# Performance work log

Measured on AMD Instinct MI355X. Metric: run time of the kernel, lower is better.

The kernel has to match this reference:

```python
import jax, jax.numpy as jnp
import numpy as np

B, N, K = 2, 8192, 9
FEAT, COST = 128, 128
LEAKY = 0.1
BN_EPS = 1e-5


def setup_inputs() -> dict:
    key = jax.random.key(0)
    ks = iter(jax.random.split(key, 64))

    def nrm(shape, s=0.05):
        return jax.random.normal(next(ks), shape, jnp.float32) * s

    inp = {
        "xyz": nrm((B, 3, N), 1.0),
        "feats": nrm((B, FEAT, N), 1.0),
        "cost_volume": nrm((B, COST, N), 1.0),
        "flow": nrm((B, 3, N), 1.0),
    }
    cin = FEAT + COST + 3  # feats + cost + flow channels = 259
    for i, (ci, co) in enumerate([(cin + 3, 128), (128 + 3, 128)]):
        p = f"pc{i}_"
        inp[p + "wn_w0"] = nrm((8, 3)); inp[p + "wn_b0"] = nrm((8,))
        inp[p + "wn_w1"] = nrm((8, 8)); inp[p + "wn_b1"] = nrm((8,))
        inp[p + "wn_w2"] = nrm((16, 8)); inp[p + "wn_b2"] = nrm((16,))
        inp[p + "lin_w"] = nrm((co, 16 * ci)); inp[p + "lin_b"] = nrm((co,))
        inp[p + "bn_g"] = 1.0 + nrm((co,)); inp[p + "bn_b"] = nrm((co,))
        inp[p + "bn_m"] = nrm((co,))
        inp[p + "bn_v"] = jax.random.uniform(next(ks), (co,), jnp.float32, 0.5, 1.5)
    inp["mlp0_w"] = nrm((128, 128)); inp["mlp0_b"] = nrm((128,))
    inp["mlp1_w"] = nrm((64, 128)); inp["mlp1_b"] = nrm((64,))
    inp["fc_w"] = nrm((3, 64)); inp["fc_b"] = nrm((3,))
    return inp


def _leaky(x):
    return jnp.where(x > 0, x, LEAKY * x)


def _pointconv(xyz, pts, wn, lin_w, lin_b, bn):
    # xyz: [B,N,3], pts: [B,N,D]
    Bn, Nn, _ = xyz.shape
    sq = jnp.sum(xyz * xyz, -1)
    # squared pairwise distances [B,N,N]
    d = sq[:, :, None] + sq[:, None, :] - 2.0 * jnp.einsum('bnc,bmc->bnm', xyz, xyz)
    _, idx = jax.lax.top_k(-d, K)  # K nearest neighbors, [B,N,K]
    gat = jax.vmap(lambda p, i: p[i])
    gxyz = gat(xyz, idx)                       # [B,N,K,3]
    norm = gxyz - xyz[:, :, None, :]           # relative coords
    gpts = gat(pts, idx)                       # [B,N,K,D]
    feat = jnp.concatenate([norm, gpts], -1)   # [B,N,K,C]
    w = norm
    for W, b in wn:  # WeightNet: 1x1 convs == per-neighbor MLP, ReLU
        w = jax.nn.relu(jnp.einsum('bnki,oi->bnko', w, W) + b)
    # aggregate: [B,N,C,K] @ [B,N,K,16] -> [B,N,C*16]
    agg = jnp.einsum('bnkc,bnkw->bncw', feat, w).reshape(Bn, Nn, -1)
    y = agg @ lin_w.T + lin_b
    g, bb, m, v = bn  # BatchNorm1d eval mode
    y = (y - m) * (g / jnp.sqrt(v + BN_EPS)) + bb
    return _leaky(y)


def reference(xyz, feats, cost_volume, flow,
              pc0_wn_w0, pc0_wn_b0, pc0_wn_w1, pc0_wn_b1, pc0_wn_w2, pc0_wn_b2,
              pc0_lin_w, pc0_lin_b, pc0_bn_g, pc0_bn_b, pc0_bn_m, pc0_bn_v,
              pc1_wn_w0, pc1_wn_b0, pc1_wn_w1, pc1_wn_b1, pc1_wn_w2, pc1_wn_b2,
              pc1_lin_w, pc1_lin_b, pc1_bn_g, pc1_bn_b, pc1_bn_m, pc1_bn_v,
              mlp0_w, mlp0_b, mlp1_w, mlp1_b, fc_w, fc_b):
    xyz_t = xyz.transpose(0, 2, 1)  # [B,N,3]
    pts = jnp.concatenate([feats, cost_volume, flow], 1).transpose(0, 2, 1)  # [B,N,259]
    pts = _pointconv(xyz_t, pts,
                     [(pc0_wn_w0, pc0_wn_b0), (pc0_wn_w1, pc0_wn_b1), (pc0_wn_w2, pc0_wn_b2)],
                     pc0_lin_w, pc0_lin_b, (pc0_bn_g, pc0_bn_b, pc0_bn_m, pc0_bn_v))
    pts = _pointconv(xyz_t, pts,
                     [(pc1_wn_w0, pc1_wn_b0), (pc1_wn_w1, pc1_wn_b1), (pc1_wn_w2, pc1_wn_b2)],
                     pc1_lin_w, pc1_lin_b, (pc1_bn_g, pc1_bn_b, pc1_bn_m, pc1_bn_v))
    pts = _leaky(pts @ mlp0_w.T + mlp0_b)
    pts = _leaky(pts @ mlp1_w.T + mlp1_b)
    fl = pts @ fc_w.T + fc_b
    return (pts.transpose(0, 2, 1), jnp.clip(fl, -200.0, 200.0).transpose(0, 2, 1))
```

## Files before the change

### kernel.cpp

```cpp
#include <hip/hip_runtime.h>
#include <hip/hip_bf16.h>
#include <stdint.h>

#define NPTS 8192
#define NB 2

typedef unsigned int uint32;
typedef unsigned long long u64;
typedef unsigned short u16;
typedef short short8 __attribute__((ext_vector_type(8)));
typedef float f32x4 __attribute__((ext_vector_type(4)));

#define WB_IDX9  6291456u
#define WB_NORM  7077888u
#define WB_WT    9175040u
#define WB_PTS1  19660800u
#define WB_PTS2  28049408u
#define WB_L0BF  36438016u
#define WB_L0LO  37519360u
#define WB_L1BF  38600704u
#define WB_L1LO  39141376u
#define WB_W0BF  39682048u
#define WB_W0LO  39714816u
#define WB_W1BF  39747584u
#define WB_W1LO  39763968u
#define WB_BN    39780352u
#define WB_KEYS  19660800u

__device__ __forceinline__ u16 f2bf(float x) {
  uint32 u = __float_as_uint(x);
  u += 0x7fffu + ((u >> 16) & 1u);
  return (u16)(u >> 16);
}
__device__ __forceinline__ float bf2f(u16 h) { return __uint_as_float((uint32)h << 16); }
__device__ __forceinline__ float lrelu(float x) { return x > 0.f ? x : 0.1f * x; }
__device__ __forceinline__ uint32 ford(float d) {
  uint32 u = __float_as_uint(d);
  return (u & 0x80000000u) ? ~u : (u | 0x80000000u);
}
__device__ __forceinline__ float unford(uint32 o) {
  return (o & 0x80000000u) ? __uint_as_float(o & 0x7FFFFFFFu) : __uint_as_float(~o);
}
__device__ __forceinline__ float sq3n(float x, float y, float z) {
  return __fadd_rn(__fadd_rn(__fmul_rn(x, x), __fmul_rn(y, y)), __fmul_rn(z, z));
}

__global__ void k_prep(const float* __restrict__ L0, const float* __restrict__ L1,
                       const float* __restrict__ W0, const float* __restrict__ W1,
                       const float* __restrict__ lb0, const float* __restrict__ g0,
                       const float* __restrict__ bb0, const float* __restrict__ m0,
                       const float* __restrict__ v0,
                       const float* __restrict__ lb1, const float* __restrict__ g1,
                       const float* __restrict__ bb1, const float* __restrict__ m1,
                       const float* __restrict__ v1,
                       u16* __restrict__ L0bf, u16* __restrict__ L0lo,
                       u16* __restrict__ L1bf, u16* __restrict__ L1lo,
                       u16* __restrict__ W0bf, u16* __restrict__ W0lo,
                       u16* __restrict__ W1bf, u16* __restrict__ W1lo,
                       float* __restrict__ bn) {
  int i = blockIdx.x * 256 + threadIdx.x;
  if (i < 128 * 4224) {
    int o = i / 4224, kk = i % 4224;
    float w = kk < 4192 ? L0[o * 4192 + kk] : 0.f;
    u16 h = f2bf(w);
    L0bf[i] = h;
    L0lo[i] = f2bf(w - bf2f(h));
    return;
  }
  i -= 128 * 4224;
  if (i < 128 * 2112) {
    int o = i / 2112, kk = i % 2112;
    float w = kk < 2096 ? L1[o * 2096 + kk] : 0.f;
    u16 h = f2bf(w);
    L1bf[i] = h;
    L1lo[i] = f2bf(w - bf2f(h));
    return;
  }
  i -= 128 * 2112;
  if (i < 16384) {
    float w = W0[i];
    u16 h = f2bf(w);
    W0bf[i] = h;
    W0lo[i] = f2bf(w - bf2f(h));
    return;
  }
  i -= 16384;
  if (i < 8192) {
    float w = W1[i];
    u16 h = f2bf(w);
    W1bf[i] = h;
    W1lo[i] = f2bf(w - bf2f(h));
    return;
  }
  i -= 8192;
  if (i < 256) {
    int layer = i >> 7, o = i & 127;
    if (layer == 0) {
      float s = g0[o] / sqrtf(v0[o] + 1e-5f);
      bn[o] = s;
      bn[128 + o] = (lb0[o] - m0[o]) * s + bb0[o];
    } else {
      float s = g1[o] / sqrtf(v1[o] + 1e-5f);
      bn[256 + o] = s;
      bn[384 + o] = (lb1[o] - m1[o]) * s + bb1[o];
    }
  }
}

__global__ __launch_bounds__(256, 2) void k_knn(const float* __restrict__ xyz,
                                                u64* __restrict__ keys) {
  __shared__ float4 cand[1024];
  int bid = blockIdx.x;
  int b = bid >> 8;
  int qt = (bid >> 3) & 31;
  int ch = bid & 7;
  const float* xb = xyz + b * 3 * NPTS;
  int c0 = ch * 1024;
  for (int t = threadIdx.x; t < 1024; t += 256) {
    int j = c0 + t;
    float x = xb[j], y = xb[NPTS + j], z = xb[2 * NPTS + j];
    cand[t] = make_float4(x, y, z, sq3n(x, y, z));
  }
  __syncthreads();
  int q = qt * 256 + threadIdx.x;
  float qx = xb[q], qy = xb[NPTS + q], qz = xb[2 * NPTS + q];
  float sqq = sq3n(qx, qy, qz);
  u64 s[10];
#pragma unroll
  for (int i = 0; i < 10; i++) s[i] = ~0ull;
#pragma unroll 2
  for (int j = 0; j < 1024; j++) {
    float4 c = cand[j];
    float dot = __fadd_rn(__fadd_rn(__fmul_rn(qx, c.x), __fmul_rn(qy, c.y)),
                          __fmul_rn(qz, c.z));
    float d = __fsub_rn(__fadd_rn(sqq, c.w), __fmul_rn(2.0f, dot));
    u64 key = ((u64)ford(d) << 13) | (uint32)(c0 + j);
    if (key < s[9]) {
      s[9] = key;
#pragma unroll
      for (int t = 9; t > 0; --t) {
        u64 a = s[t - 1], bq = s[t];
        s[t - 1] = a < bq ? a : bq;
        s[t] = a < bq ? bq : a;
      }
    }
  }
  u64* dst = keys + ((size_t)(b * NPTS + q) * 8 + ch) * 10;
#pragma unroll
  for (int i = 0; i < 10; i++) dst[i] = s[i];
}

__global__ __launch_bounds__(256) void k_merge(const u64* __restrict__ keys,
                                               int* __restrict__ idx9) {
  int t = blockIdx.x * 256 + threadIdx.x;
  const u64* src = keys + (size_t)t * 80;
  u64 s[10];
#pragma unroll
  for (int i = 0; i < 10; i++) s[i] = ~0ull;
  for (int g = 0; g < 8; g++) {
#pragma unroll
    for (int i = 0; i < 10; i++) {
      u64 k = src[g * 10 + i];
      if (k >= s[9]) break;
      s[9] = k;
#pragma unroll
      for (int j = 9; j > 0; --j) {
        u64 a = s[j - 1], bq = s[j];
        s[j - 1] = a < bq ? a : bq;
        s[j] = a < bq ? bq : a;
      }
    }
  }
  float d8 = unford((uint32)(s[8] >> 13));
  float d9 = unford((uint32)(s[9] >> 13));
  int amb = (d9 - d8) < 1.5e-6f ? 1 : 0;
  int* dst = idx9 + (size_t)t * 12;
#pragma unroll
  for (int i = 0; i < 10; i++) dst[i] = (int)(s[i] & 8191u);
  dst[10] = amb;
}

__global__ __launch_bounds__(256) void k_wn(const float* __restrict__ xyz,
                                            const int* __restrict__ idx9,
                                            const float* __restrict__ w0, const float* __restrict__ b0,
                                            const float* __restrict__ w1, const float* __restrict__ b1,
                                            const float* __restrict__ w2, const float* __restrict__ b2,
                                            float* __restrict__ norm_ws, float* __restrict__ wt_ws) {
  __shared__ float sw0[24], sb0[8], sw1[64], sb1[8], sw2[128], sb2[16];
  int tid = threadIdx.x;
  if (tid < 24) sw0[tid] = w0[tid];
  if (tid < 8) { sb0[tid] = b0[tid]; sb1[tid] = b1[tid]; }
  if (tid < 64) sw1[tid] = w1[tid];
  if (tid < 128) sw2[tid] = w2[tid];
  if (tid < 16) sb2[tid] = b2[tid];
  __syncthreads();
  int t = blockIdx.x * 256 + tid;
  if (t >= NB * NPTS * 10) return;
  int b = t / (NPTS * 10);
  int r = t % (NPTS * 10);
  int n = r / 10, k = r % 10;
  const float* xb = xyz + b * 3 * NPTS;
  const int* row = idx9 + (size_t)(b * NPTS + n) * 12;
  int ni = row[k];
  int amb = row[10];
  float scale = (k < 8) ? 1.f : (k == 8 ? (amb ? 0.5f : 1.f) : (amb ? 0.5f : 0.f));
  float nx = xb[ni] - xb[n];
  float ny = xb[NPTS + ni] - xb[NPTS + n];
  float nz = xb[2 * NPTS + ni] - xb[2 * NPTS + n];
  float* np = norm_ws + (size_t)(b * NPTS + n) * 32 + k * 3;
  np[0] = nx; np[1] = ny; np[2] = nz;
  float h0[8], h1[8];
#pragma unroll
  for (int o = 0; o < 8; o++) {
    float s = fmaf(sw0[o * 3], nx, fmaf(sw0[o * 3 + 1], ny, fmaf(sw0[o * 3 + 2], nz, sb0[o])));
    h0[o] = fmaxf(s, 0.f);
  }
#pragma unroll
  for (int o = 0; o < 8; o++) {
    float s = sb1[o];
#pragma unroll
    for (int i = 0; i < 8; i++) s = fmaf(sw1[o * 8 + i], h0[i], s);
    h1[o] = fmaxf(s, 0.f);
  }
  float* wp = wt_ws + (size_t)(b * NPTS + n) * 160 + k * 16;
#pragma unroll
  for (int o = 0; o < 16; o++) {
    float s = sb2[o];
#pragma unroll
    for (int i = 0; i < 8; i++) s = fmaf(sw2[o * 8 + i], h1[i], s);
    wp[o] = fmaxf(s, 0.f) * scale;
  }
}

template <int LAYER>
__global__ __launch_bounds__(256, 2) void k_conv(
    const float* __restrict__ feats, const float* __restrict__ cost,
    const float* __restrict__ flow, const float* __restrict__ pts1cm,
    const float* __restrict__ norm_ws, const float* __restrict__ wt_ws,
    const int* __restrict__ idx9, const u16* __restrict__ Lbf,
    const u16* __restrict__ Llo, const float* __restrict__ bn,
    float* __restrict__ outp) {
  constexpr int NCH = (LAYER == 0) ? 66 : 33;
  constexpr int CC = (LAYER == 0) ? 262 : 131;
  constexpr int KP = (LAYER == 0) ? 4224 : 2112;
  __shared__ int idx_s[32][10];
  __shared__ union {
    struct {
      float gf[32][40];
      u16 Ah[32][72]; u16 Al[32][72];
      u16 Bh[128][72]; u16 Bl[128][72];
    } ph;
    float yt[32][128];
  } u;
  int tid = threadIdx.x;
  int bid = blockIdx.x;
  int b = bid >> 8, n0 = (bid & 255) * 32;
  for (int t = tid; t < 320; t += 256)
    idx_s[t / 10][t % 10] = idx9[(size_t)(b * NPTS + n0 + t / 10) * 12 + t % 10];
  int p_a = tid >> 3;
  int w0i = (tid & 7) * 2;
  float wr0[10], wr1[10];
  {
    const float* wp = wt_ws + (size_t)(b * NPTS + n0 + p_a) * 160 + w0i;
#pragma unroll
    for (int k = 0; k < 10; k++) {
      float2 v = *(const float2*)(wp + k * 16);
      wr0[k] = v.x; wr1[k] = v.y;
    }
  }
  __syncthreads();
  int lane = tid & 63, wv = tid >> 6;
  int pg = wv >> 1, oh = wv & 1;
  f32x4 acc0 = {0.f, 0.f, 0.f, 0.f}, acc1 = acc0, acc2 = acc0, acc3 = acc0;

  for (int chq = 0; chq < NCH; chq++) {
    int c0 = chq * 4;
    for (int v = tid; v < 1280; v += 256) {
      int p = v / 40, r = v % 40, k = r >> 2, cl = r & 3;
      int c = c0 + cl;
      float val = 0.f;
      int ni = idx_s[p][k];
      if (c < 3)
        val = norm_ws[(size_t)(b * NPTS + n0 + p) * 32 + k * 3 + c];
      else if (c < CC) {
        int cc = c - 3;
        if (LAYER == 0) {
          if (cc < 128) val = feats[(size_t)(b * 128 + cc) * NPTS + ni];
          else if (cc < 256) val = cost[(size_t)(b * 128 + cc - 128) * NPTS + ni];
          else val = flow[(size_t)(b * 3 + cc - 256) * NPTS + ni];
        } else {
          val = pts1cm[(size_t)(b * 128 + cc) * NPTS + ni];
        }
      }
      u.ph.gf[p][r] = val;
    }
    __syncthreads();
#pragma unroll
    for (int cl = 0; cl < 4; cl++) {
      float a0 = 0.f, a1 = 0.f;
#pragma unroll
      for (int k = 0; k < 10; k++) {
        float g = u.ph.gf[p_a][k * 4 + cl];
        a0 = fmaf(g, wr0[k], a0);
        a1 = fmaf(g, wr1[k], a1);
      }
      u16 h0 = f2bf(a0);
      u16 l0 = f2bf(a0 - bf2f(h0));
      u16 h1 = f2bf(a1);
      u16 l1 = f2bf(a1 - bf2f(h1));
      *(uint32*)&u.ph.Ah[p_a][cl * 16 + w0i] = (uint32)h0 | ((uint32)h1 << 16);
      *(uint32*)&u.ph.Al[p_a][cl * 16 + w0i] = (uint32)l0 | ((uint32)l1 << 16);
    }
    {
      int o = tid >> 1, half = tid & 1;
      const uint4* s4 = (const uint4*)(Lbf + (size_t)o * KP + c0 * 16 + half * 32);
      const uint4* s4l = (const uint4*)(Llo + (size_t)o * KP + c0 * 16 + half * 32);
      uint4* d4 = (uint4*)&u.ph.Bh[o][half * 32];
      uint4* d4l = (uint4*)&u.ph.Bl[o][half * 32];
      d4[0] = s4[0]; d4[1] = s4[1]; d4[2] = s4[2]; d4[3] = s4[3];
      d4l[0] = s4l[0]; d4l[1] = s4l[1]; d4l[2] = s4l[2]; d4l[3] = s4l[3];
    }
    __syncthreads();
    {
      int arow = pg * 16 + (lane & 15);
      int koff = (lane >> 4) * 8;
      int brow = (lane & 15);
#pragma unroll
      for (int ks = 0; ks < 2; ks++) {
        short8 ah = *(const short8*)&u.ph.Ah[arow][ks * 32 + koff];
        short8 al = *(const short8*)&u.ph.Al[arow][ks * 32 + koff];
        short8 b0v = *(const short8*)&u.ph.Bh[(oh * 4 + 0) * 16 + brow][ks * 32 + koff];
        short8 b0l = *(const short8*)&u.ph.Bl[(oh * 4 + 0) * 16 + brow][ks * 32 + koff];
        acc0 = __builtin_amdgcn_mfma_f32_16x16x32_bf16(ah, b0v, acc0, 0, 0, 0);
        acc0 = __builtin_amdgcn_mfma_f32_16x16x32_bf16(al, b0v, acc0, 0, 0, 0);
        acc0 = __builtin_amdgcn_mfma_f32_16x16x32_bf16(ah, b0l, acc0, 0, 0, 0);
        short8 b1v = *(const short8*)&u.ph.Bh[(oh * 4 + 1) * 16 + brow][ks * 32 + koff];
        short8 b1l = *(const short8*)&u.ph.Bl[(oh * 4 + 1) * 16 + brow][ks * 32 + koff];
        acc1 = __builtin_amdgcn_mfma_f32_16x16x32_bf16(ah, b1v, acc1, 0, 0, 0);
        acc1 = __builtin_amdgcn_mfma_f32_16x16x32_bf16(al, b1v, acc1, 0, 0, 0);
        acc1 = __builtin_amdgcn_mfma_f32_16x16x32_bf16(ah, b1l, acc1, 0, 0, 0);
        short8 b2v = *(const short8*)&u.ph.Bh[(oh * 4 + 2) * 16 + brow][ks * 32 + koff];
        short8 b2l = *(const short8*)&u.ph.Bl[(oh * 4 + 2) * 16 + brow][ks * 32 + koff];
        acc2 = __builtin_amdgcn_mfma_f32_16x16x32_bf16(ah, b2v, acc2, 0, 0, 0);
        acc2 = __builtin_amdgcn_mfma_f32_16x16x32_bf16(al, b2v, acc2, 0, 0, 0);
        acc2 = __builtin_amdgcn_mfma_f32_16x16x32_bf16(ah, b2l, acc2, 0, 0, 0);
        short8 b3v = *(const short8*)&u.ph.Bh[(oh * 4 + 3) * 16 + brow][ks * 32 + koff];
        short8 b3l = *(const short8*)&u.ph.Bl[(oh * 4 + 3) * 16 + brow][ks * 32 + koff];
        acc3 = __builtin_amdgcn_mfma_f32_16x16x32_bf16(ah, b3v, acc3, 0, 0, 0);
        acc3 = __builtin_amdgcn_mfma_f32_16x16x32_bf16(al, b3v, acc3, 0, 0, 0);
        acc3 = __builtin_amdgcn_mfma_f32_16x16x32_bf16(ah, b3l, acc3, 0, 0, 0);
      }
    }
    __syncthreads();
  }
  const float* sc = bn;
  const float* sh = bn + 128;
  int prow = pg * 16 + (lane >> 4) * 4;
  if (LAYER == 0) {
#pragma unroll
    for (int t = 0; t < 4; t++) {
      int o = (oh * 4 + t) * 16 + (lane & 15);
      float s = sc[o], h = sh[o];
      f32x4 a = (t == 0) ? acc0 : (t == 1) ? acc1 : (t == 2) ? acc2 : acc3;
#pragma unroll
      for (int r = 0; r < 4; r++) u.yt[prow + r][o] = lrelu(fmaf(a[r], s, h));
    }
    __syncthreads();
    int o = tid >> 1, pq = (tid & 1) * 16;
    float* dst = outp + (size_t)(b * 128 + o) * NPTS + n0 + pq;
#pragma unroll
    for (int i = 0; i < 16; i += 4) {
      float4 vv = make_float4(u.yt[pq + i][o], u.yt[pq + i + 1][o],
                              u.yt[pq + i + 2][o], u.yt[pq + i + 3][o]);
      *(float4*)(dst + i) = vv;
    }
  } else {
#pragma unroll
    for (int t = 0; t < 4; t++) {
      int o = (oh * 4 + t) * 16 + (lane & 15);
      float s = sc[o], h = sh[o];
      f32x4 a = (t == 0) ? acc0 : (t == 1) ? acc1 : (t == 2) ? acc2 : acc3;
#pragma unroll
      for (int r = 0; r < 4; r++)
        outp[(size_t)(b * NPTS + n0 + prow + r) * 128 + o] = lrelu(fmaf(a[r], s, h));
    }
  }
}

__global__ __launch_bounds__(256) void k_mlp(const float* __restrict__ pts2,
                                             const u16* __restrict__ W0bf,
                                             const u16* __restrict__ W0lo,
                                             const u16* __restrict__ W1bf,
                                             const u16* __restrict__ W1lo,
                                             const float* __restrict__ b0,
                                             const float* __restrict__ b1,
                                             const float* __restrict__ fcw,
                                             const float* __restrict__ fcb,
                                             float* __restrict__ out0,
                                             float* __restrict__ out1) {
  __shared__ u16 A_s[32][136];
  __shared__ u16 Al_s[32][136];
  __shared__ u16 W_s[128][136];
  __shared__ float yt[32][68];
  int tid = threadIdx.x;
  int b = blockIdx.x >> 8, n0 = (blockIdx.x & 255) * 32;
  {
    int p = tid >> 3, cq = (tid & 7) * 16;
    const float* src = pts2 + (size_t)(b * NPTS + n0 + p) * 128 + cq;
#pragma unroll
    for (int i = 0; i < 16; i++) {
      float x = src[i];
      u16 h = f2bf(x);
      A_s[p][cq + i] = h;
      Al_s[p][cq + i] = f2bf(x - bf2f(h));
    }
  }
  {
    int o = tid >> 1, half = tid & 1;
    const uint4* s4 = (const uint4*)(W0bf + o * 128 + half * 64);
    uint4* d4 = (uint4*)&W_s[o][half * 64];
#pragma unroll
    for (int i = 0; i < 8; i++) d4[i] = s4[i];
  }
  __syncthreads();
  int lane = tid & 63, wv = tid >> 6, pg = wv >> 1, oh = wv & 1;
  int arow = pg * 16 + (lane & 15), koff = (lane >> 4) * 8, brow = lane & 15;
  int prow = pg * 16 + (lane >> 4) * 4;
  f32x4 y0a = {0.f, 0.f, 0.f, 0.f}, y0b = y0a, y0c = y0a, y0d = y0a;
#pragma unroll
  for (int ks = 0; ks < 4; ks++) {
    short8 af = *(const short8*)&A_s[arow][ks * 32 + koff];
    short8 afl = *(const short8*)&Al_s[arow][ks * 32 + koff];
    short8 w0v = *(const short8*)&W_s[(oh * 4 + 0) * 16 + brow][ks * 32 + koff];
    y0a = __builtin_amdgcn_mfma_f32_16x16x32_bf16(af, w0v, y0a, 0, 0, 0);
    y0a = __builtin_amdgcn_mfma_f32_16x16x32_bf16(afl, w0v, y0a, 0, 0, 0);
    short8 w1v = *(const short8*)&W_s[(oh * 4 + 1) * 16 + brow][ks * 32 + koff];
    y0b = __builtin_amdgcn_mfma_f32_16x16x32_bf16(af, w1v, y0b, 0, 0, 0);
    y0b = __builtin_amdgcn_mfma_f32_16x16x32_bf16(afl, w1v, y0b, 0, 0, 0);
    short8 w2v = *(const short8*)&W_s[(oh * 4 + 2) * 16 + brow][ks * 32 + koff];
    y0c = __builtin_amdgcn_mfma_f32_16x16x32_bf16(af, w2v, y0c, 0, 0, 0);
    y0c = __builtin_amdgcn_mfma_f32_16x16x32_bf16(afl, w2v, y0c, 0, 0, 0);
    short8 w3v = *(const short8*)&W_s[(oh * 4 + 3) * 16 + brow][ks * 32 + koff];
    y0d = __builtin_amdgcn_mfma_f32_16x16x32_bf16(af, w3v, y0d, 0, 0, 0);
    y0d = __builtin_amdgcn_mfma_f32_16x16x32_bf16(afl, w3v, y0d, 0, 0, 0);
  }
  __syncthreads();
  {
    int o = tid >> 1, half = tid & 1;
    const uint4* s4 = (const uint4*)(W0lo + o * 128 + half * 64);
    uint4* d4 = (uint4*)&W_s[o][half * 64];
#pragma unroll
    for (int i = 0; i < 8; i++) d4[i] = s4[i];
  }
  __syncthreads();
#pragma unroll
  for (int ks = 0; ks < 4; ks++) {
    short8 af = *(const short8*)&A_s[arow][ks * 32 + koff];
    short8 w0v = *(const short8*)&W_s[(oh * 4 + 0) * 16 + brow][ks * 32 + koff];
    y0a = __builtin_amdgcn_mfma_f32_16x16x32_bf16(af, w0v, y0a, 0, 0, 0);
    short8 w1v = *(const short8*)&W_s[(oh * 4 + 1) * 16 + brow][ks * 32 + koff];
    y0b = __builtin_amdgcn_mfma_f32_16x16x32_bf16(af, w1v, y0b, 0, 0, 0);
    short8 w2v = *(const short8*)&W_s[(oh * 4 + 2) * 16 + brow][ks * 32 + koff];
    y0c = __builtin_amdgcn_mfma_f32_16x16x32_bf16(af, w2v, y0c, 0, 0, 0);
    short8 w3v = *(const short8*)&W_s[(oh * 4 + 3) * 16 + brow][ks * 32 + koff];
    y0d = __builtin_amdgcn_mfma_f32_16x16x32_bf16(af, w3v, y0d, 0, 0, 0);
  }
  __syncthreads();
#pragma unroll
  for (int t = 0; t < 4; t++) {
    int o = (oh * 4 + t) * 16 + (lane & 15);
    float bias = b0[o];
    f32x4 a = (t == 0) ? y0a : (t == 1) ? y0b : (t == 2) ? y0c : y0d;
#pragma unroll
    for (int r = 0; r < 4; r++) {
      float x = lrelu(a[r] + bias);
      u16 h = f2bf(x);
      A_s[prow + r][o] = h;
      Al_s[prow + r][o] = f2bf(x - bf2f(h));
    }
  }
  {
    int o = tid >> 2, qq = (tid & 3) * 32;
    const uint4* s4 = (const uint4*)(W1bf + o * 128 + qq);
    uint4* d4 = (uint4*)&W_s[o][qq];
#pragma unroll
    for (int i = 0; i < 4; i++) d4[i] = s4[i];
  }
  __syncthreads();
  f32x4 y1a = {0.f, 0.f, 0.f, 0.f}, y1b = y1a;
#pragma unroll
  for (int ks = 0; ks < 4; ks++) {
    short8 af = *(const short8*)&A_s[arow][ks * 32 + koff];
    short8 afl = *(const short8*)&Al_s[arow][ks * 32 + koff];
    short8 w0v = *(const short8*)&W_s[(oh * 2 + 0) * 16 + brow][ks * 32 + koff];
    y1a = __builtin_amdgcn_mfma_f32_16x16x32_bf16(af, w0v, y1a, 0, 0, 0);
    y1a = __builtin_amdgcn_mfma_f32_16x16x32_bf16(afl, w0v, y1a, 0, 0, 0);
    short8 w1v = *(const short8*)&W_s[(oh * 2 + 1) * 16 + brow][ks * 32 + koff];
    y1b = __builtin_amdgcn_mfma_f32_16x16x32_bf16(af, w1v, y1b, 0, 0, 0);
    y1b = __builtin_amdgcn_mfma_f32_16x16x32_bf16(afl, w1v, y1b, 0, 0, 0);
  }
  __syncthreads();
  {
    int o = tid >> 2, qq = (tid & 3) * 32;
    const uint4* s4 = (const uint4*)(W1lo + o * 128 + qq);
    uint4* d4 = (uint4*)&W_s[o][qq];
#pragma unroll
    for (int i = 0; i < 4; i++) d4[i] = s4[i];
  }
  __syncthreads();
#pragma unroll
  for (int ks = 0; ks < 4; ks++) {
    short8 af = *(const short8*)&A_s[arow][ks * 32 + koff];
    short8 w0v = *(const short8*)&W_s[(oh * 2 + 0) * 16 + brow][ks * 32 + koff];
    y1a = __builtin_amdgcn_mfma_f32_16x16x32_bf16(af, w0v, y1a, 0, 0, 0);
    short8 w1v = *(const short8*)&W_s[(oh * 2 + 1) * 16 + brow][ks * 32 + koff];
    y1b = __builtin_amdgcn_mfma_f32_16x16x32_bf16(af, w1v, y1b, 0, 0, 0);
  }
#pragma unroll
  for (int t = 0; t < 2; t++) {
    int o = (oh * 2 + t) * 16 + (lane & 15);
    float bias = b1[o];
    f32x4 a = t ? y1b : y1a;
#pragma unroll
    for (int r = 0; r < 4; r++) yt[prow + r][o] = lrelu(a[r] + bias);
  }
  __syncthreads();
  {
    int o = tid >> 2, pq = (tid & 3) * 8;
    float* dst = out0 + (size_t)(b * 64 + o) * NPTS + n0 + pq;
#pragma unroll
    for (int i = 0; i < 8; i += 4) {
      float4 vv = make_float4(yt[pq + i][o], yt[pq + i + 1][o],
                              yt[pq + i + 2][o], yt[pq + i + 3][o]);
      *(float4*)(dst + i) = vv;
    }
  }
  if (tid < 96) {
    int p = tid / 3, j = tid % 3;
    float s = fcb[j];
#pragma unroll
    for (int c = 0; c < 64; c++) s = fmaf(fcw[j * 64 + c], yt[p][c], s);
    s = fminf(fmaxf(s, -200.f), 200.f);
    out1[(size_t)(b * 3 + j) * NPTS + n0 + p] = s;
  }
}

extern "C" void kernel_launch(void* const* d_in, const int* in_sizes, int n_in,
                              void* d_out, int out_size, void* d_ws, size_t ws_size,
                              hipStream_t stream) {
  const float* xyz = (const float*)d_in[0];
  const float* feats = (const float*)d_in[1];
  const float* cost = (const float*)d_in[2];
  const float* flow = (const float*)d_in[3];
  const float* p0w0 = (const float*)d_in[4];
  const float* p0b0 = (const float*)d_in[5];
  const float* p0w1 = (const float*)d_in[6];
  const float* p0b1 = (const float*)d_in[7];
  const float* p0w2 = (const float*)d_in[8];
  const float* p0b2 = (const float*)d_in[9];
  const float* p0lw = (const float*)d_in[10];
  const float* p0lb = (const float*)d_in[11];
  const float* p0g = (const float*)d_in[12];
  const float* p0bb = (const float*)d_in[13];
  const float* p0m = (const float*)d_in[14];
  const float* p0v = (const float*)d_in[15];
  const float* p1w0 = (const float*)d_in[16];
  const float* p1b0 = (const float*)d_in[17];
  const float* p1w1 = (const float*)d_in[18];
  const float* p1b1 = (const float*)d_in[19];
  const float* p1w2 = (const float*)d_in[20];
  const float* p1b2 = (const float*)d_in[21];
  const float* p1lw = (const float*)d_in[22];
  const float* p1lb = (const float*)d_in[23];
  const float* p1g = (const float*)d_in[24];
  const float* p1bb = (const float*)d_in[25];
  const float* p1m = (const float*)d_in[26];
  const float* p1v = (const float*)d_in[27];
  const float* m0w = (const float*)d_in[28];
  const float* m0b = (const float*)d_in[29];
  const float* m1w = (const float*)d_in[30];
  const float* m1b = (const float*)d_in[31];
  const float* fcw = (const float*)d_in[32];
  const float* fcb = (const float*)d_in[33];

  char* ws = (char*)d_ws;
  u64* keys = (u64*)(ws + WB_KEYS);
  int* idx9 = (int*)(ws + WB_IDX9);
  float* norm_ws = (float*)(ws + WB_NORM);
  float* wt_ws = (float*)(ws + WB_WT);
  float* pts1 = (float*)(ws + WB_PTS1);
  float* pts2 = (float*)(ws + WB_PTS2);
  u16* L0bf = (u16*)(ws + WB_L0BF);
  u16* L0lo = (u16*)(ws + WB_L0LO);
  u16* L1bf = (u16*)(ws + WB_L1BF);
  u16* L1lo = (u16*)(ws + WB_L1LO);
  u16* W0bf = (u16*)(ws + WB_W0BF);
  u16* W0lo = (u16*)(ws + WB_W0LO);
  u16* W1bf = (u16*)(ws + WB_W1BF);
  u16* W1lo = (u16*)(ws + WB_W1LO);
  float* bn = (float*)(ws + WB_BN);

  k_knn<<<512, 256, 0, stream>>>(xyz, keys);
  k_merge<<<64, 256, 0, stream>>>(keys, idx9);
  k_prep<<<3265, 256, 0, stream>>>(p0lw, p1lw, m0w, m1w, p0lb, p0g, p0bb, p0m, p0v,
                                   p1lb, p1g, p1bb, p1m, p1v,
                                   L0bf, L0lo, L1bf, L1lo, W0bf, W0lo, W1bf, W1lo, bn);
  k_wn<<<640, 256, 0, stream>>>(xyz, idx9, p0w0, p0b0, p0w1, p0b1, p0w2, p0b2, norm_ws, wt_ws);
  k_conv<0><<<512, 256, 0, stream>>>(feats, cost, flow, nullptr, norm_ws, wt_ws, idx9,
                                     L0bf, L0lo, bn, pts1);
  k_wn<<<640, 256, 0, stream>>>(xyz, idx9, p1w0, p1b0, p1w1, p1b1, p1w2, p1b2, norm_ws, wt_ws);
  k_conv<1><<<512, 256, 0, stream>>>(feats, cost, flow, pts1, norm_ws, wt_ws, idx9,
                                     L1bf, L1lo, bn + 256, pts2);
  k_mlp<<<512, 256, 0, stream>>>(pts2, W0bf, W0lo, W1bf, W1lo, m0b, m1b, fcw, fcb,
                                 (float*)d_out, (float*)d_out + (size_t)2 * 64 * NPTS);
}
```

Measured before the change: 815.9 us.

## Software-pipeline gather and weight loads through registers; single shared B buffer

Restructures the k_conv main loop so the neighbor-feature gather and the bf16 hi/lo weight tiles are prefetched into registers one or two chunks ahead, overlapping global latency with MFMA work. The separate Bh/Bl shared buffers become one Bx buffer, reused for the hi and lo weight passes in turn. This cuts shared memory and may raise occupancy. The cost is more registers, an extra barrier per chunk, and index precomputation held in registers.

```diff
diff --git a/kernel.cpp b/kernel.cpp
--- a/kernel.cpp
+++ b/kernel.cpp
@@ -248,7 +248,7 @@
     struct {
       float gf[32][40];
       u16 Ah[32][72]; u16 Al[32][72];
-      u16 Bh[128][72]; u16 Bl[128][72];
+      u16 Bx[128][72];
     } ph;
     float yt[32][128];
   } u;
@@ -269,32 +269,74 @@
     }
   }
   __syncthreads();
+
+  int sp[5], sk[5], scl[5], sni[5], soff[5];
+#pragma unroll
+  for (int j = 0; j < 5; j++) {
+    int v = tid + j * 256;
+    int p = v / 40, r = v % 40;
+    sp[j] = p; soff[j] = r;
+    sk[j] = r >> 2; scl[j] = r & 3;
+    sni[j] = idx_s[p][sk[j]];
+  }
+  int bo = tid >> 1, bhalf = tid & 1;
+
   int lane = tid & 63, wv = tid >> 6;
   int pg = wv >> 1, oh = wv & 1;
+  int arow = pg * 16 + (lane & 15);
+  int koff = (lane >> 4) * 8;
+  int brow = lane & 15;
   f32x4 acc0 = {0.f, 0.f, 0.f, 0.f}, acc1 = acc0, acc2 = acc0, acc3 = acc0;
 
+  float rG[5];
+  uint4 rBh[4], rBl[4];
+
+#define GATHER_TO(C0) \
+  _Pragma("unroll") \
+  for (int j = 0; j < 5; j++) { \
+    int c = (C0) + scl[j]; \
+    float val = 0.f; \
+    int ni = sni[j]; \
+    if (c < 3) \
+      val = norm_ws[(size_t)(b * NPTS + n0 + sp[j]) * 32 + sk[j] * 3 + c]; \
+    else if (c < CC) { \
+      int cc = c - 3; \
+      if (LAYER == 0) { \
+        if (cc < 128) val = feats[(size_t)(b * 128 + cc) * NPTS + ni]; \
+        else if (cc < 256) val = cost[(size_t)(b * 128 + cc - 128) * NPTS + ni]; \
+        else val = flow[(size_t)(b * 3 + cc - 256) * NPTS + ni]; \
+      } else { \
+        val = pts1cm[(size_t)(b * 128 + cc) * NPTS + ni]; \
+      } \
+    } \
+    rG[j] = val; \
+  }
+
+#define LOADB(SRC, REGS, C0) { \
+    const uint4* s4_ = (const uint4*)((SRC) + (size_t)bo * KP + (C0) * 16 + bhalf * 32); \
+    REGS[0] = s4_[0]; REGS[1] = s4_[1]; REGS[2] = s4_[2]; REGS[3] = s4_[3]; }
+
+#define WRITEB(REGS) { \
+    uint4* d4_ = (uint4*)&u.ph.Bx[bo][bhalf * 32]; \
+    d4_[0] = REGS[0]; d4_[1] = REGS[1]; d4_[2] = REGS[2]; d4_[3] = REGS[3]; }
+
+#define WRITEG() { \
+    _Pragma("unroll") \
+    for (int j = 0; j < 5; j++) u.ph.gf[sp[j]][soff[j]] = rG[j]; }
+
+  GATHER_TO(0)
+  LOADB(Lbf, rBh, 0)
+  LOADB(Llo, rBl, 0)
+  WRITEG()
+  WRITEB(rBh)
+  {
+    int nq = (1 < NCH) ? 1 : NCH - 1;
+    GATHER_TO(nq * 4)
+    LOADB(Lbf, rBh, nq * 4)
+  }
+  __syncthreads();
+
   for (int chq = 0; chq < NCH; chq++) {
-    int c0 = chq * 4;
-    for (int v = tid; v < 1280; v += 256) {
-      int p = v / 40, r = v % 40, k = r >> 2, cl = r & 3;
-      int c = c0 + cl;
-      float val = 0.f;
-      int ni = idx_s[p][k];
-      if (c < 3)
-        val = norm_ws[(size_t)(b * NPTS + n0 + p) * 32 + k * 3 + c];
-      else if (c < CC) {
-        int cc = c - 3;
-        if (LAYER == 0) {
-          if (cc < 128) val = feats[(size_t)(b * 128 + cc) * NPTS + ni];
-          else if (cc < 256) val = cost[(size_t)(b * 128 + cc - 128) * NPTS + ni];
-          else val = flow[(size_t)(b * 3 + cc - 256) * NPTS + ni];
-        } else {
-          val = pts1cm[(size_t)(b * 128 + cc) * NPTS + ni];
-        }
-      }
-      u.ph.gf[p][r] = val;
-    }
-    __syncthreads();
 #pragma unroll
     for (int cl = 0; cl < 4; cl++) {
       float a0 = 0.f, a1 = 0.f;
@@ -311,48 +353,58 @@
       *(uint32*)&u.ph.Ah[p_a][cl * 16 + w0i] = (uint32)h0 | ((uint32)h1 << 16);
       *(uint32*)&u.ph.Al[p_a][cl * 16 + w0i] = (uint32)l0 | ((uint32)l1 << 16);
     }
+    __syncthreads();
+#pragma unroll
+    for (int ks = 0; ks < 2; ks++) {
+      short8 ah = *(const short8*)&u.ph.Ah[arow][ks * 32 + koff];
+      short8 al = *(const short8*)&u.ph.Al[arow][ks * 32 + koff];
+      short8 b0v = *(const short8*)&u.ph.Bx[(oh * 4 + 0) * 16 + brow][ks * 32 + koff];
+      acc0 = __builtin_amdgcn_mfma_f32_16x16x32_bf16(ah, b0v, acc0, 0, 0, 0);
+      acc0 = __builtin_amdgcn_mfma_f32_16x16x32_bf16(al, b0v, acc0, 0, 0, 0);
+      short8 b1v = *(const short8*)&u.ph.Bx[(oh * 4 + 1) * 16 + brow][ks * 32 + koff];
+      acc1 = __builtin_amdgcn_mfma_f32_16x16x32_bf16(ah, b1v, acc1, 0, 0, 0);
+      acc1 = __builtin_amdgcn_mfma_f32_16x16x32_bf16(al, b1v, acc1, 0, 0, 0);
+      short8 b2v = *(const short8*)&u.ph.Bx[(oh * 4 + 2) * 16 + brow][ks * 32 + koff];
+      acc2 = __builtin_amdgcn_mfma_f32_16x16x32_bf16(ah, b2v, acc2, 0, 0, 0);
+      acc2 = __builtin_amdgcn_mfma_f32_16x16x32_bf16(al, b2v, acc2, 0, 0, 0);
+      short8 b3v = *(const short8*)&u.ph.Bx[(oh * 4 + 3) * 16 + brow][ks * 32 + koff];
+      acc3 = __builtin_amdgcn_mfma_f32_16x16x32_bf16(ah, b3v, acc3, 0, 0, 0);
+      acc3 = __builtin_amdgcn_mfma_f32_16x16x32_bf16(al, b3v, acc3, 0, 0, 0);
+    }
+    __syncthreads();
+    WRITEB(rBl)
+    WRITEG()
     {
-      int o = tid >> 1, half = tid & 1;
-      const uint4* s4 = (const uint4*)(Lbf + (size_t)o * KP + c0 * 16 + half * 32);
-      const uint4* s4l = (const uint4*)(Llo + (size_t)o * KP + c0 * 16 + half * 32);
-      uint4* d4 = (uint4*)&u.ph.Bh[o][half * 32];
-      uint4* d4l = (uint4*)&u.ph.Bl[o][half * 32];
-      d4[0] = s4[0]; d4[1] = s4[1]; d4[2] = s4[2]; d4[3] = s4[3];
-      d4l[0] = s4l[0]; d4l[1] = s4l[1]; d4l[2] = s4l[2]; d4l[3] = s4l[3];
+      int nq = (chq + 1 < NCH) ? chq + 1 : NCH - 1;
+      LOADB(Llo, rBl, nq * 4)
+      int nq2 = (chq + 2 < NCH) ? chq + 2 : NCH - 1;
+      GATHER_TO(nq2 * 4)
     }
     __syncthreads();
-    {
-      int arow = pg * 16 + (lane & 15);
-      int koff = (lane >> 4) * 8;
-      int brow = (lane & 15);
-#pragma unroll
-      for (int ks = 0; ks < 2; ks++) {
-        short8 ah = *(const short8*)&u.ph.Ah[arow][ks * 32 + koff];
-        short8 al = *(const short8*)&u.ph.Al[arow][ks * 32 + koff];
-        short8 b0v = *(const short8*)&u.ph.Bh[(oh * 4 + 0) * 16 + brow][ks * 32 + koff];
-        short8 b0l = *(const short8*)&u.ph.Bl[(oh * 4 + 0) * 16 + brow][ks * 32 + koff];
-        acc0 = __builtin_amdgcn_mfma_f32_16x16x32_bf16(ah, b0v, acc0, 0, 0, 0);
-        acc0 = __builtin_amdgcn_mfma_f32_16x16x32_bf16(al, b0v, acc0, 0, 0, 0);
-        acc0 = __builtin_amdgcn_mfma_f32_16x16x32_bf16(ah, b0l, acc0, 0, 0, 0);
-        short8 b1v = *(const short8*)&u.ph.Bh[(oh * 4 + 1) * 16 + brow][ks * 32 + koff];
-        short8 b1l = *(const short8*)&u.ph.Bl[(oh * 4 + 1) * 16 + brow][ks * 32 + koff];
-        acc1 = __builtin_amdgcn_mfma_f32_16x16x32_bf16(ah, b1v, acc1, 0, 0, 0);
-        acc1 = __builtin_amdgcn_mfma_f32_16x16x32_bf16(al, b1v, acc1, 0, 0, 0);
-        acc1 = __builtin_amdgcn_mfma_f32_16x16x32_bf16(ah, b1l, acc1, 0, 0, 0);
-        short8 b2v = *(const short8*)&u.ph.Bh[(oh * 4 + 2) * 16 + brow][ks * 32 + koff];
-        short8 b2l = *(const short8*)&u.ph.Bl[(oh * 4 + 2) * 16 + brow][ks * 32 + koff];
-        acc2 = __builtin_amdgcn_mfma_f32_16x16x32_bf16(ah, b2v, acc2, 0, 0, 0);
-        acc2 = __builtin_amdgcn_mfma_f32_16x16x32_bf16(al, b2v, acc2, 0, 0, 0);
-        acc2 = __builtin_amdgcn_mfma_f32_16x16x32_bf16(ah, b2l, acc2, 0, 0, 0);
-        short8 b3v = *(const short8*)&u.ph.Bh[(oh * 4 + 3) * 16 + brow][ks * 32 + koff];
-        short8 b3l = *(const short8*)&u.ph.Bl[(oh * 4 + 3) * 16 + brow][ks * 32 + koff];
-        acc3 = __builtin_amdgcn_mfma_f32_16x16x32_bf16(ah, b3v, acc3, 0, 0, 0);
-        acc3 = __builtin_amdgcn_mfma_f32_16x16x32_bf16(al, b3v, acc3, 0, 0, 0);
-        acc3 = __builtin_amdgcn_mfma_f32_16x16x32_bf16(ah, b3l, acc3, 0, 0, 0);
-      }
+#pragma unroll
+    for (int ks = 0; ks < 2; ks++) {
+      short8 ah = *(const short8*)&u.ph.Ah[arow][ks * 32 + koff];
+      short8 b0v = *(const short8*)&u.ph.Bx[(oh * 4 + 0) * 16 + brow][ks * 32 + koff];
+      acc0 = __builtin_amdgcn_mfma_f32_16x16x32_bf16(ah, b0v, acc0, 0, 0, 0);
+      short8 b1v = *(const short8*)&u.ph.Bx[(oh * 4 + 1) * 16 + brow][ks * 32 + koff];
+      acc1 = __builtin_amdgcn_mfma_f32_16x16x32_bf16(ah, b1v, acc1, 0, 0, 0);
+      short8 b2v = *(const short8*)&u.ph.Bx[(oh * 4 + 2) * 16 + brow][ks * 32 + koff];
+      acc2 = __builtin_amdgcn_mfma_f32_16x16x32_bf16(ah, b2v, acc2, 0, 0, 0);
+      short8 b3v = *(const short8*)&u.ph.Bx[(oh * 4 + 3) * 16 + brow][ks * 32 + koff];
+      acc3 = __builtin_amdgcn_mfma_f32_16x16x32_bf16(ah, b3v, acc3, 0, 0, 0);
     }
     __syncthreads();
-  }
+    if (chq + 1 < NCH) {
+      WRITEB(rBh)
+      int nq3 = (chq + 2 < NCH) ? chq + 2 : NCH - 1;
+      LOADB(Lbf, rBh, nq3 * 4)
+    }
+  }
+#undef GATHER_TO
+#undef LOADB
+#undef WRITEB
+#undef WRITEG
+
   const float* sc = bn;
   const float* sh = bn + 128;
   int prow = pg * 16 + (lane >> 4) * 4;
```

Measured after the change: 1.030 ms. 26.2% more time.
